# Kernel optimization log

Measured on AMD Instinct MI355X. Metric: run time of the kernel, lower is better.

Reference implementation:

```python
import jax, jax.numpy as jnp
import numpy as np

B, S, H, HD = 8, 1024, 16, 64
D = H * HD
NINF = -10000.0
EPS = 1e-6


def setup_inputs() -> dict:
    key = jax.random.key(0)
    ks = jax.random.split(key, 6)
    std = 0.02
    return {
        "x": jax.random.normal(ks[0], (B, S, D), jnp.float32),
        "mask": jax.random.randint(ks[1], (B, S), 0, 2, jnp.int32),
        "wq": jax.random.normal(ks[2], (D, D), jnp.float32) * std,
        "bq": jnp.zeros((D,), jnp.float32),
        "wk": jax.random.normal(ks[3], (D, D), jnp.float32) * std,
        "bk": jnp.zeros((D,), jnp.float32),
        "wv": jax.random.normal(ks[4], (D, D), jnp.float32) * std,
        "bv": jnp.zeros((D,), jnp.float32),
        "wo": jax.random.normal(ks[5], (D, D), jnp.float32) * std,
        "bo": jnp.zeros((D,), jnp.float32),
        "gamma": jnp.ones((D,), jnp.float32),
        "beta": jnp.zeros((D,), jnp.float32),
    }


def _heads(t):
    # [B,S,D] -> [B,H,S,HD]
    return t.reshape(t.shape[0], t.shape[1], H, HD).transpose(0, 2, 1, 3)


def _layernorm(x, gamma, beta):
    mu = jnp.mean(x, -1, keepdims=True)
    var = jnp.mean(jnp.square(x - mu), -1, keepdims=True)
    return (x - mu) * jax.lax.rsqrt(var + EPS) * gamma + beta


def reference(x, mask, wq, bq, wk, bk, wv, bv, wo, bo, gamma, beta):
    q = _heads(x @ wq + bq)
    k = _heads(x @ wk + bk)
    v = _heads(x @ wv + bv)
    scores = jnp.einsum("bhqd,bhkd->bhqk", q, k) / np.sqrt(HD).astype(np.float32)
    # padding mask broadcast over key axis: 1 = masked
    scores = scores + mask.astype(jnp.float32)[:, None, None, :] * NINF
    attn = jax.nn.softmax(scores, axis=-1)
    ctx = jnp.einsum("bhqk,bhkd->bhqd", attn, v)  # [B,H,S,HD]
    ctx = ctx.transpose(0, 2, 1, 3).reshape(B, S, D)
    out = _layernorm(x + ctx @ wo + bo, gamma, beta)
    return out
```

## Files before the change

kernel.cpp:

```cpp
#include <hip/hip_runtime.h>
#include <stdint.h>

typedef unsigned short u16;
typedef unsigned int u32;
typedef __bf16 b16x8 __attribute__((ext_vector_type(8)));
typedef float f32x4 __attribute__((ext_vector_type(4)));

#define B_ 8
#define S_ 1024
#define H_ 16
#define HD_ 64
#define D_ 1024
#define M_ 8192

__device__ __forceinline__ u16 f2bf(float f) {
  u32 u = __float_as_uint(f);
  return (u16)((u + 0x7fffu + ((u >> 16) & 1u)) >> 16);
}

__device__ __forceinline__ f32x4 mfma16(b16x8 a, b16x8 b, f32x4 c) {
  return __builtin_amdgcn_mfma_f32_16x16x32_bf16(a, b, c, 0, 0, 0);
}

__device__ __forceinline__ void cp16(const u16* g, u16* l) {
  __builtin_amdgcn_global_load_lds(
      (const __attribute__((address_space(1))) u32*)(g),
      (__attribute__((address_space(3))) u32*)(l), 16, 0, 0);
}

__global__ __launch_bounds__(1024) void wconv_kernel(
    const float* __restrict__ w0, const float* __restrict__ w1,
    const float* __restrict__ w2, const float* __restrict__ w3,
    u16* __restrict__ t0, u16* __restrict__ t1, u16* __restrict__ t2,
    u16* __restrict__ t3) {
  __shared__ float tile[32][33];
  const int z = blockIdx.z;
  const float* src = (z == 0) ? w0 : (z == 1) ? w1 : (z == 2) ? w2 : w3;
  u16* dst = (z == 0) ? t0 : (z == 1) ? t1 : (z == 2) ? t2 : t3;
  const int tx = threadIdx.x, ty = threadIdx.y;
  const int x0 = blockIdx.x * 32, y0 = blockIdx.y * 32;
  tile[ty][tx] = src[(size_t)(y0 + ty) * D_ + x0 + tx];
  __syncthreads();
  dst[(size_t)(x0 + ty) * D_ + y0 + tx] = f2bf(tile[tx][ty]);
}

__global__ __launch_bounds__(256) void xconv_kernel(const float* __restrict__ x,
                                                    u16* __restrict__ xb) {
  const size_t i = ((size_t)blockIdx.x * 256 + threadIdx.x) * 4;
  const float4 v = *(const float4*)(x + i);
  u16 o[4] = {f2bf(v.x), f2bf(v.y), f2bf(v.z), f2bf(v.w)};
  uint2 pack;
  pack.x = ((u32)o[1] << 16) | o[0];
  pack.y = ((u32)o[3] << 16) | o[2];
  *(uint2*)(xb + i) = pack;
}

__device__ __forceinline__ void gemm128_mainloop(
    const u16* __restrict__ A, const u16* __restrict__ BT, int K, int m0,
    int n0, u16* lds, f32x4 (&acc)[4][4]) {
  const int t = threadIdx.x;
  const int lane = t & 63;
  const int w = t >> 6;
  const int l15 = lane & 15;
  const int q4 = lane >> 4;
  const int mwave = (w >> 1) * 64;
  const int nwave = (w & 1) * 64;

  u16* Alds = lds;
  u16* Blds = lds + 8192;

  const f32x4 zero = {0.f, 0.f, 0.f, 0.f};
  for (int mt = 0; mt < 4; ++mt)
    for (int nt = 0; nt < 4; ++nt) acc[mt][nt] = zero;

  const int rbase = t >> 3;
  const int scol = ((t & 7) ^ (rbase & 7)) * 8;
  const u16* Ag = A + (size_t)(m0 + rbase) * K + scol;
  const u16* Bg = BT + (size_t)(n0 + rbase) * K + scol;

  const int sx = l15 & 7;
  const int cA0 = ((0 * 4 + q4) ^ sx) * 8;
  const int cA1 = ((1 * 4 + q4) ^ sx) * 8;

  for (int k0 = 0; k0 < K; k0 += 64) {
    __syncthreads();
    for (int c = 0; c < 4; ++c) {
      cp16(Ag + (size_t)(c * 32) * K + k0, Alds + c * 2048 + t * 8);
      cp16(Bg + (size_t)(c * 32) * K + k0, Blds + c * 2048 + t * 8);
    }
    __syncthreads();

    b16x8 af[4][2], bfr[4][2];
    for (int mt = 0; mt < 4; ++mt) {
      const int row = (mwave + mt * 16 + l15) * 64;
      af[mt][0] = *(const b16x8*)(Alds + row + cA0);
      af[mt][1] = *(const b16x8*)(Alds + row + cA1);
    }
    for (int nt = 0; nt < 4; ++nt) {
      const int row = (nwave + nt * 16 + l15) * 64;
      bfr[nt][0] = *(const b16x8*)(Blds + row + cA0);
      bfr[nt][1] = *(const b16x8*)(Blds + row + cA1);
    }
    for (int mt = 0; mt < 4; ++mt)
      for (int nt = 0; nt < 4; ++nt) {
        acc[mt][nt] = mfma16(af[mt][0], bfr[nt][0], acc[mt][nt]);
        acc[mt][nt] = mfma16(af[mt][1], bfr[nt][1], acc[mt][nt]);
      }
  }
}

__global__ __launch_bounds__(256) void qkv_gemm_kernel(
    const u16* __restrict__ xb, const u16* __restrict__ wtq,
    const u16* __restrict__ wtk, const u16* __restrict__ wtv,
    const float* __restrict__ bq, const float* __restrict__ bk,
    const float* __restrict__ bv, u16* __restrict__ Q, u16* __restrict__ Kb,
    u16* __restrict__ VT) {
  __shared__ __align__(16) u16 lds[16384];
  const int z = blockIdx.z;
  const u16* BTp = (z == 0) ? wtq : (z == 1) ? wtk : wtv;
  const float* bias = (z == 0) ? bq : (z == 1) ? bk : bv;
  u16* out = (z == 0) ? Q : (z == 1) ? Kb : VT;
  const int m0 = blockIdx.y * 128, n0 = blockIdx.x * 128;

  f32x4 acc[4][4];
  gemm128_mainloop(xb, BTp, D_, m0, n0, lds, acc);

  const int lane = threadIdx.x & 63, w = threadIdx.x >> 6;
  const int l15 = lane & 15, q4 = lane >> 4;
  const int mwave = (w >> 1) * 64, nwave = (w & 1) * 64;

  for (int nt = 0; nt < 4; ++nt) {
    const int n = n0 + nwave + nt * 16 + l15;
    const float bias_v = bias[n];
    const int h = n >> 6, hd = n & 63;
    for (int mt = 0; mt < 4; ++mt) {
      for (int r = 0; r < 4; ++r) {
        const int m = m0 + mwave + mt * 16 + q4 * 4 + r;
        const int b = m >> 10, s = m & 1023;
        const float v = acc[mt][nt][r] + bias_v;
        size_t idx;
        if (z < 2)
          idx = (((size_t)(b * H_ + h)) * S_ + s) * HD_ + hd;
        else
          idx = (((size_t)(b * H_ + h)) * HD_ + hd) * S_ + s;
        out[idx] = f2bf(v);
      }
    }
  }
}

#define PAD_ 68
__global__ __launch_bounds__(256) void attn_kernel(
    const u16* __restrict__ Q, const u16* __restrict__ Kb,
    const u16* __restrict__ VT, const int* __restrict__ mask,
    u16* __restrict__ ctx) {
  __shared__ __align__(16) u16 QPlds[64 * PAD_];
  __shared__ __align__(16) u16 Klds[64 * PAD_];
  __shared__ __align__(16) u16 Vlds[64 * PAD_];
  __shared__ __align__(16) float Mlds[1024];

  const int t = threadIdx.x;
  const int lane = t & 63, w = t >> 6;
  const int l15 = lane & 15, q4 = lane >> 4;
  const int bh = blockIdx.y;
  const int b = bh >> 4, h = bh & 15;
  const int q0 = blockIdx.x * 64;

  const u16* Qbh = Q + (size_t)bh * S_ * HD_;
  const u16* Kbh = Kb + (size_t)bh * S_ * HD_;
  const u16* Vbh = VT + (size_t)bh * S_ * HD_;
  const int* maskb = mask + b * S_;

  const int srow = t >> 3, scol = (t & 7) * 8;
  {
    b16x8 q0v = *(const b16x8*)(Qbh + (size_t)(q0 + srow) * HD_ + scol);
    b16x8 q1v = *(const b16x8*)(Qbh + (size_t)(q0 + srow + 32) * HD_ + scol);
    const int4 mv = *(const int4*)(maskb + t * 4);
    *(b16x8*)(QPlds + srow * PAD_ + scol) = q0v;
    *(b16x8*)(QPlds + (srow + 32) * PAD_ + scol) = q1v;
    float4 mf;
    mf.x = -14427.0f * (float)mv.x;
    mf.y = -14427.0f * (float)mv.y;
    mf.z = -14427.0f * (float)mv.z;
    mf.w = -14427.0f * (float)mv.w;
    *(float4*)(Mlds + t * 4) = mf;
  }
  __syncthreads();
  b16x8 aq[2];
  aq[0] = *(const b16x8*)(QPlds + (w * 16 + l15) * PAD_ + q4 * 8);
  aq[1] = *(const b16x8*)(QPlds + (w * 16 + l15) * PAD_ + 32 + q4 * 8);

  const f32x4 zero = {0.f, 0.f, 0.f, 0.f};
  f32x4 acc[4];
  for (int nt = 0; nt < 4; ++nt) acc[nt] = zero;
  float lsum[4] = {0.f, 0.f, 0.f, 0.f};
  u16* Pw = QPlds + w * 16 * PAD_;
  const float c1 = 0.18033688f;

  b16x8 kv0 = *(const b16x8*)(Kbh + (size_t)srow * HD_ + scol);
  b16x8 kv1 = *(const b16x8*)(Kbh + (size_t)(srow + 32) * HD_ + scol);
  b16x8 vv0 = *(const b16x8*)(Vbh + (size_t)srow * S_ + scol);
  b16x8 vv1 = *(const b16x8*)(Vbh + (size_t)(srow + 32) * S_ + scol);

  for (int j = 0; j < 16; ++j) {
    const int key0 = j * 64;
    __syncthreads();
    *(b16x8*)(Klds + srow * PAD_ + scol) = kv0;
    *(b16x8*)(Klds + (srow + 32) * PAD_ + scol) = kv1;
    *(b16x8*)(Vlds + srow * PAD_ + scol) = vv0;
    *(b16x8*)(Vlds + (srow + 32) * PAD_ + scol) = vv1;
    __syncthreads();

    if (j < 15) {
      const int kn = key0 + 64;
      kv0 = *(const b16x8*)(Kbh + (size_t)(kn + srow) * HD_ + scol);
      kv1 = *(const b16x8*)(Kbh + (size_t)(kn + srow + 32) * HD_ + scol);
      vv0 = *(const b16x8*)(Vbh + (size_t)srow * S_ + kn + scol);
      vv1 = *(const b16x8*)(Vbh + (size_t)(srow + 32) * S_ + kn + scol);
    }

    float madd[4];
    for (int nt = 0; nt < 4; ++nt) madd[nt] = Mlds[key0 + nt * 16 + l15];

    f32x4 sf[4];
    for (int nt = 0; nt < 4; ++nt) sf[nt] = zero;
    for (int kk = 0; kk < 2; ++kk)
      for (int nt = 0; nt < 4; ++nt) {
        b16x8 bk =
            *(const b16x8*)(Klds + (nt * 16 + l15) * PAD_ + kk * 32 + q4 * 8);
        sf[nt] = mfma16(aq[kk], bk, sf[nt]);
      }

    for (int nt = 0; nt < 4; ++nt)
      for (int r = 0; r < 4; ++r) {
        const float p = __builtin_amdgcn_exp2f(sf[nt][r] * c1 + madd[nt]);
        lsum[r] += p;
        *(__bf16*)(Pw + (q4 * 4 + r) * PAD_ + nt * 16 + l15) = (__bf16)p;
      }
    asm volatile("s_waitcnt lgkmcnt(0)" ::: "memory");

    for (int kk = 0; kk < 2; ++kk) {
      b16x8 ap = *(const b16x8*)(Pw + l15 * PAD_ + kk * 32 + q4 * 8);
      for (int nt = 0; nt < 4; ++nt) {
        b16x8 vb =
            *(const b16x8*)(Vlds + (nt * 16 + l15) * PAD_ + kk * 32 + q4 * 8);
        acc[nt] = mfma16(ap, vb, acc[nt]);
      }
    }
  }

  for (int r = 0; r < 4; ++r) {
    for (int off = 1; off < 16; off <<= 1) lsum[r] += __shfl_xor(lsum[r], off);
    lsum[r] = 1.0f / lsum[r];
  }

  for (int nt = 0; nt < 4; ++nt) {
    const int dcol = h * 64 + nt * 16 + l15;
    for (int r = 0; r < 4; ++r) {
      const int srw = q0 + w * 16 + q4 * 4 + r;
      const float o = acc[nt][r] * lsum[r];
      ctx[((size_t)(b * S_ + srw)) * D_ + dcol] = f2bf(o);
    }
  }
}

__global__ __launch_bounds__(256) void out_gemm_kernel(
    const u16* __restrict__ ctx, const u16* __restrict__ wto,
    const float* __restrict__ bo, const float* __restrict__ x,
    float* __restrict__ y) {
  __shared__ __align__(16) u16 lds[16384];
  const int m0 = blockIdx.y * 128, n0 = blockIdx.x * 128;
  f32x4 acc[4][4];
  gemm128_mainloop(ctx, wto, D_, m0, n0, lds, acc);

  const int lane = threadIdx.x & 63, w = threadIdx.x >> 6;
  const int l15 = lane & 15, q4 = lane >> 4;
  const int mwave = (w >> 1) * 64, nwave = (w & 1) * 64;

  for (int nt = 0; nt < 4; ++nt) {
    const int n = n0 + nwave + nt * 16 + l15;
    const float bias = bo[n];
    for (int mt = 0; mt < 4; ++mt) {
      for (int r = 0; r < 4; ++r) {
        const int m = m0 + mwave + mt * 16 + q4 * 4 + r;
        y[(size_t)m * D_ + n] = acc[mt][nt][r] + bias + x[(size_t)m * D_ + n];
      }
    }
  }
}

__global__ __launch_bounds__(256) void ln_kernel(const float* __restrict__ y,
                                                 const float* __restrict__ g,
                                                 const float* __restrict__ be,
                                                 float* __restrict__ out) {
  const int row = blockIdx.x, t = threadIdx.x;
  const float* yr = y + (size_t)row * D_;
  const float4 v = *(const float4*)(yr + t * 4);
  float s = v.x + v.y + v.z + v.w;
  float ss = v.x * v.x + v.y * v.y + v.z * v.z + v.w * v.w;
  for (int off = 1; off < 64; off <<= 1) {
    s += __shfl_xor(s, off);
    ss += __shfl_xor(ss, off);
  }
  __shared__ float red[8];
  const int w = t >> 6, lane = t & 63;
  if (lane == 0) {
    red[w] = s;
    red[4 + w] = ss;
  }
  __syncthreads();
  s = red[0] + red[1] + red[2] + red[3];
  ss = red[4] + red[5] + red[6] + red[7];
  const float mu = s * (1.f / 1024.f);
  const float var = ss * (1.f / 1024.f) - mu * mu;
  const float rs = rsqrtf(var + 1e-6f);
  const int c = t * 4;
  const float4 gv = *(const float4*)(g + c);
  const float4 bv = *(const float4*)(be + c);
  float4 o;
  o.x = (v.x - mu) * rs * gv.x + bv.x;
  o.y = (v.y - mu) * rs * gv.y + bv.y;
  o.z = (v.z - mu) * rs * gv.z + bv.z;
  o.w = (v.w - mu) * rs * gv.w + bv.w;
  *(float4*)(out + (size_t)row * D_ + c) = o;
}

extern "C" void kernel_launch(void* const* d_in, const int* in_sizes, int n_in,
                              void* d_out, int out_size, void* d_ws,
                              size_t ws_size, hipStream_t stream) {
  const float* x = (const float*)d_in[0];
  const int* mask = (const int*)d_in[1];
  const float* wq = (const float*)d_in[2];
  const float* bq = (const float*)d_in[3];
  const float* wk = (const float*)d_in[4];
  const float* bk = (const float*)d_in[5];
  const float* wv = (const float*)d_in[6];
  const float* bv = (const float*)d_in[7];
  const float* wo = (const float*)d_in[8];
  const float* bo = (const float*)d_in[9];
  const float* gamma = (const float*)d_in[10];
  const float* beta = (const float*)d_in[11];
  float* out = (float*)d_out;

  char* ws = (char*)d_ws;
  const size_t MB = 1024ull * 1024ull;
  u16* wtq = (u16*)(ws + 0 * MB);
  u16* wtk = (u16*)(ws + 2 * MB);
  u16* wtv = (u16*)(ws + 4 * MB);
  u16* wto = (u16*)(ws + 6 * MB);
  u16* xb = (u16*)(ws + 8 * MB);
  u16* ctx = (u16*)(ws + 8 * MB);
  u16* Qb = (u16*)(ws + 24 * MB);
  u16* Kb = (u16*)(ws + 40 * MB);
  u16* VTb = (u16*)(ws + 56 * MB);
  float* y = (float*)(ws + 24 * MB);

  wconv_kernel<<<dim3(32, 32, 4), dim3(32, 32), 0, stream>>>(
      wq, wk, wv, wo, wtq, wtk, wtv, wto);
  xconv_kernel<<<8192, 256, 0, stream>>>(x, xb);
  qkv_gemm_kernel<<<dim3(8, 64, 3), 256, 0, stream>>>(
      xb, wtq, wtk, wtv, bq, bk, bv, Qb, Kb, VTb);
  attn_kernel<<<dim3(16, 128), 256, 0, stream>>>(Qb, Kb, VTb, mask, ctx);
  out_gemm_kernel<<<dim3(8, 64), 256, 0, stream>>>(ctx, wto, bo, x, y);
  ln_kernel<<<8192, 256, 0, stream>>>(y, gamma, beta, out);
}
```

Baseline: 337.1 us.

## Transpose attention MFMA operands to vectorize P stores and ctx writes

```diff
diff --git a/kernel.cpp b/kernel.cpp
--- a/kernel.cpp
+++ b/kernel.cpp
@@ -16,6 +16,14 @@
 __device__ __forceinline__ u16 f2bf(float f) {
   u32 u = __float_as_uint(f);
   return (u16)((u + 0x7fffu + ((u >> 16) & 1u)) >> 16);
+}
+__device__ __forceinline__ u16 bfbits(float f) {
+  union {
+    __bf16 b;
+    u16 u;
+  } c;
+  c.b = (__bf16)f;
+  return c.u;
 }
 
 __device__ __forceinline__ f32x4 mfma16(b16x8 a, b16x8 b, f32x4 c) {
@@ -150,11 +158,12 @@
 }
 
 #define PAD_ 68
+#define QPAD_ 72
 __global__ __launch_bounds__(256) void attn_kernel(
     const u16* __restrict__ Q, const u16* __restrict__ Kb,
     const u16* __restrict__ VT, const int* __restrict__ mask,
     u16* __restrict__ ctx) {
-  __shared__ __align__(16) u16 QPlds[64 * PAD_];
+  __shared__ __align__(16) u16 QPlds[64 * QPAD_];
   __shared__ __align__(16) u16 Klds[64 * PAD_];
   __shared__ __align__(16) u16 Vlds[64 * PAD_];
   __shared__ __align__(16) float Mlds[1024];
@@ -162,9 +171,10 @@
   const int t = threadIdx.x;
   const int lane = t & 63, w = t >> 6;
   const int l15 = lane & 15, q4 = lane >> 4;
-  const int bh = blockIdx.y;
+  const int id = blockIdx.x;
+  const int bh = id & 127;
   const int b = bh >> 4, h = bh & 15;
-  const int q0 = blockIdx.x * 64;
+  const int q0 = (id >> 7) * 64;
 
   const u16* Qbh = Q + (size_t)bh * S_ * HD_;
   const u16* Kbh = Kb + (size_t)bh * S_ * HD_;
@@ -176,8 +186,8 @@
     b16x8 q0v = *(const b16x8*)(Qbh + (size_t)(q0 + srow) * HD_ + scol);
     b16x8 q1v = *(const b16x8*)(Qbh + (size_t)(q0 + srow + 32) * HD_ + scol);
     const int4 mv = *(const int4*)(maskb + t * 4);
-    *(b16x8*)(QPlds + srow * PAD_ + scol) = q0v;
-    *(b16x8*)(QPlds + (srow + 32) * PAD_ + scol) = q1v;
+    *(b16x8*)(QPlds + srow * QPAD_ + scol) = q0v;
+    *(b16x8*)(QPlds + (srow + 32) * QPAD_ + scol) = q1v;
     float4 mf;
     mf.x = -14427.0f * (float)mv.x;
     mf.y = -14427.0f * (float)mv.y;
@@ -187,14 +197,14 @@
   }
   __syncthreads();
   b16x8 aq[2];
-  aq[0] = *(const b16x8*)(QPlds + (w * 16 + l15) * PAD_ + q4 * 8);
-  aq[1] = *(const b16x8*)(QPlds + (w * 16 + l15) * PAD_ + 32 + q4 * 8);
+  aq[0] = *(const b16x8*)(QPlds + (w * 16 + l15) * QPAD_ + q4 * 8);
+  aq[1] = *(const b16x8*)(QPlds + (w * 16 + l15) * QPAD_ + 32 + q4 * 8);
 
   const f32x4 zero = {0.f, 0.f, 0.f, 0.f};
   f32x4 acc[4];
   for (int nt = 0; nt < 4; ++nt) acc[nt] = zero;
-  float lsum[4] = {0.f, 0.f, 0.f, 0.f};
-  u16* Pw = QPlds + w * 16 * PAD_;
+  float lsum = 0.f;
+  u16* Pw = QPlds + w * 16 * QPAD_;
   const float c1 = 0.18033688f;
 
   b16x8 kv0 = *(const b16x8*)(Kbh + (size_t)srow * HD_ + scol);
@@ -219,48 +229,50 @@
       vv1 = *(const b16x8*)(Vbh + (size_t)(srow + 32) * S_ + kn + scol);
     }
 
-    float madd[4];
-    for (int nt = 0; nt < 4; ++nt) madd[nt] = Mlds[key0 + nt * 16 + l15];
-
     f32x4 sf[4];
     for (int nt = 0; nt < 4; ++nt) sf[nt] = zero;
     for (int kk = 0; kk < 2; ++kk)
       for (int nt = 0; nt < 4; ++nt) {
         b16x8 bk =
             *(const b16x8*)(Klds + (nt * 16 + l15) * PAD_ + kk * 32 + q4 * 8);
-        sf[nt] = mfma16(aq[kk], bk, sf[nt]);
-      }
-
-    for (int nt = 0; nt < 4; ++nt)
-      for (int r = 0; r < 4; ++r) {
-        const float p = __builtin_amdgcn_exp2f(sf[nt][r] * c1 + madd[nt]);
-        lsum[r] += p;
-        *(__bf16*)(Pw + (q4 * 4 + r) * PAD_ + nt * 16 + l15) = (__bf16)p;
-      }
+        sf[nt] = mfma16(bk, aq[kk], sf[nt]);
+      }
+
+    for (int nt = 0; nt < 4; ++nt) {
+      const float4 mk = *(const float4*)(Mlds + key0 + nt * 16 + q4 * 4);
+      float p0 = __builtin_amdgcn_exp2f(sf[nt][0] * c1 + mk.x);
+      float p1 = __builtin_amdgcn_exp2f(sf[nt][1] * c1 + mk.y);
+      float p2 = __builtin_amdgcn_exp2f(sf[nt][2] * c1 + mk.z);
+      float p3 = __builtin_amdgcn_exp2f(sf[nt][3] * c1 + mk.w);
+      lsum += (p0 + p1) + (p2 + p3);
+      uint2 pk;
+      pk.x = ((u32)bfbits(p1) << 16) | bfbits(p0);
+      pk.y = ((u32)bfbits(p3) << 16) | bfbits(p2);
+      *(uint2*)(Pw + l15 * QPAD_ + nt * 16 + q4 * 4) = pk;
+    }
     asm volatile("s_waitcnt lgkmcnt(0)" ::: "memory");
 
     for (int kk = 0; kk < 2; ++kk) {
-      b16x8 ap = *(const b16x8*)(Pw + l15 * PAD_ + kk * 32 + q4 * 8);
+      b16x8 bp = *(const b16x8*)(Pw + l15 * QPAD_ + kk * 32 + q4 * 8);
       for (int nt = 0; nt < 4; ++nt) {
         b16x8 vb =
             *(const b16x8*)(Vlds + (nt * 16 + l15) * PAD_ + kk * 32 + q4 * 8);
-        acc[nt] = mfma16(ap, vb, acc[nt]);
-      }
-    }
-  }
-
-  for (int r = 0; r < 4; ++r) {
-    for (int off = 1; off < 16; off <<= 1) lsum[r] += __shfl_xor(lsum[r], off);
-    lsum[r] = 1.0f / lsum[r];
-  }
-
+        acc[nt] = mfma16(vb, bp, acc[nt]);
+      }
+    }
+  }
+
+  lsum += __shfl_xor(lsum, 16);
+  lsum += __shfl_xor(lsum, 32);
+  const float inv = 1.0f / lsum;
+
+  const int srw = q0 + w * 16 + l15;
+  u16* crow = ctx + ((size_t)(b * S_ + srw)) * D_ + h * 64;
   for (int nt = 0; nt < 4; ++nt) {
-    const int dcol = h * 64 + nt * 16 + l15;
-    for (int r = 0; r < 4; ++r) {
-      const int srw = q0 + w * 16 + q4 * 4 + r;
-      const float o = acc[nt][r] * lsum[r];
-      ctx[((size_t)(b * S_ + srw)) * D_ + dcol] = f2bf(o);
-    }
+    uint2 pk;
+    pk.x = ((u32)bfbits(acc[nt][1] * inv) << 16) | bfbits(acc[nt][0] * inv);
+    pk.y = ((u32)bfbits(acc[nt][3] * inv) << 16) | bfbits(acc[nt][2] * inv);
+    *(uint2*)(crow + nt * 16 + q4 * 4) = pk;
   }
 }
 
@@ -360,7 +372,7 @@
   xconv_kernel<<<8192, 256, 0, stream>>>(x, xb);
   qkv_gemm_kernel<<<dim3(8, 64, 3), 256, 0, stream>>>(
       xb, wtq, wtk, wtv, bq, bk, bv, Qb, Kb, VTb);
-  attn_kernel<<<dim3(16, 128), 256, 0, stream>>>(Qb, Kb, VTb, mask, ctx);
+  attn_kernel<<<2048, 256, 0, stream>>>(Qb, Kb, VTb, mask, ctx);
   out_gemm_kernel<<<dim3(8, 64), 256, 0, stream>>>(ctx, wto, bo, x, y);
   ln_kernel<<<8192, 256, 0, stream>>>(y, gamma, beta, out);
 }
```

Result: faster. 312.1 us (-7.4%).
